# Performance work log

Hardware: AMD Instinct MI355X
Metric: run time of the kernel (lower is better)

The kernel has to match this reference:

```python
import jax, jax.numpy as jnp
import numpy as np

N = 500000
D = 112
H = 64
W = 176


def setup_inputs() -> dict:
    key = jax.random.key(0)
    k1, k2 = jax.random.split(key)
    # positions: x in [0, W-1), y in [0, H-1)
    u = jax.random.uniform(k1, (N, 2), dtype=jnp.float32)
    sampling_positions = u * jnp.array([W - 1.0, H - 1.0], dtype=jnp.float32)
    sampling_depth_features = jax.random.normal(k2, (N, D), dtype=jnp.float32)
    return {
        "sampling_positions": sampling_positions,
        "sampling_depth_features": sampling_depth_features,
        "height": H,
        "width": W,
    }


def _bilinear_scatter(positions, features, height, width):
    # positions: [N,2] (x, y); features: [N,D] -> grid [H,W,D]
    x = positions[:, 0]
    y = positions[:, 1]
    x0 = jnp.floor(x)
    y0 = jnp.floor(y)
    wx = x - x0
    wy = y - y0
    x0i = x0.astype(jnp.int32)
    y0i = y0.astype(jnp.int32)
    x1i = x0i + 1
    y1i = y0i + 1

    out = jnp.zeros((height, width, features.shape[1]), dtype=jnp.float32)

    def in_bounds(yi, xi):
        return (yi >= 0) & (yi < height) & (xi >= 0) & (xi < width)

    corners = [
        (y0i, x0i, (1.0 - wy) * (1.0 - wx)),
        (y0i, x1i, (1.0 - wy) * wx),
        (y1i, x0i, wy * (1.0 - wx)),
        (y1i, x1i, wy * wx),
    ]
    for yi, xi, w in corners:
        valid = in_bounds(yi, xi)
        w = jnp.where(valid, w, 0.0)
        yi = jnp.clip(yi, 0, height - 1)
        xi = jnp.clip(xi, 0, width - 1)
        out = out.at[yi, xi].add(w[:, None] * features)
    return out


def reference(sampling_positions, sampling_depth_features, height, width):
    return _bilinear_scatter(sampling_positions, sampling_depth_features, height, width)
```

## Files before the change

kernel.cpp:

```cpp
#include <hip/hip_runtime.h>


#define D     112
#define H     64
#define W     176
#define HW    (H * W)
#define CAP   128
#define CSTR  16
#define TY    4
#define TX    4
#define GX    (W / TX)
#define GY    (H / TY)
#define NCELL (TY * TX)

__global__ __launch_bounds__(256) void fill_kernel(
    const float2* __restrict__ pos,
    int* __restrict__ cnt,
    uint2* __restrict__ bucket,
    int N)
{
    int p = blockIdx.x * blockDim.x + threadIdx.x;
    if (p >= N) return;

    float2 xy = pos[p];
    float xf = floorf(xy.x), yf = floorf(xy.y);
    float wx = xy.x - xf,    wy = xy.y - yf;
    int x0 = (int)xf, y0 = (int)yf;
    x0 = min(max(x0, 0), W - 1);
    y0 = min(max(y0, 0), H - 1);

    int bin = y0 * W + x0;
    unsigned qw = (__float2uint_rn(wy * 65535.0f) << 16)
                |  __float2uint_rn(wx * 65535.0f);

    int i = atomicAdd(&cnt[bin * CSTR], 1);
    if (i < CAP) bucket[(size_t)bin * CAP + i] = make_uint2((unsigned)p, qw);
}

__global__ __launch_bounds__(256) void accum_kernel(
    const float* __restrict__ feat,
    const int* __restrict__ cnt,
    const uint2* __restrict__ bucket,
    float* __restrict__ out)
{
    const int tile = blockIdx.x;
    const int ty0  = (tile / GX) * TY;
    const int tx0  = (tile % GX) * TX;
    const int t    = threadIdx.x;
    const int g    = t >> 7;
    const int tl   = t & 127;

    __shared__ uint2 se[CAP];
    __shared__ float sacc[NCELL][D];

    float acc[NCELL];
#pragma unroll
    for (int c = 0; c < NCELL; ++c) acc[c] = 0.0f;

#pragma unroll
    for (int by = -1; by < TY; ++by) {
#pragma unroll
        for (int bx = -1; bx < TX; ++bx) {
            const int gby = ty0 + by;
            const int gbx = tx0 + bx;
            int n = 0;
            if (gby >= 0 && gbx >= 0 && gbx < W)
                n = min(cnt[(gby * W + gbx) * CSTR], CAP);

            if (t < n) se[t] = bucket[(size_t)(gby * W + gbx) * CAP + t];
            __syncthreads();

            if (tl < D) {
#pragma unroll 4
                for (int e = g; e < n; e += 2) {
                    uint2 en = se[e];
                    float wx = (float)(en.y & 0xffffu) * (1.0f / 65535.0f);
                    float wy = (float)(en.y >> 16)     * (1.0f / 65535.0f);
                    float f  = feat[(size_t)en.x * D + tl];
                    float ax = 1.0f - wx, ay = 1.0f - wy;
#pragma unroll
                    for (int dy = 0; dy < 2; ++dy) {
                        const int cy = by + dy;
                        if (cy < 0 || cy >= TY) continue;
                        float fy = dy ? wy : ay;
#pragma unroll
                        for (int dx = 0; dx < 2; ++dx) {
                            const int cx = bx + dx;
                            if (cx < 0 || cx >= TX) continue;
                            float fx = dx ? wx : ax;
                            acc[cy * TX + cx] = fmaf(fy * fx, f, acc[cy * TX + cx]);
                        }
                    }
                }
            }
            __syncthreads();
        }
    }

    if (g == 1 && tl < D) {
#pragma unroll
        for (int c = 0; c < NCELL; ++c) sacc[c][tl] = acc[c];
    }
    __syncthreads();
    if (g == 0 && tl < D) {
#pragma unroll
        for (int c = 0; c < NCELL; ++c) {
            const int cy = c / TX, cx = c % TX;
            out[((size_t)(ty0 + cy) * W + (tx0 + cx)) * D + tl]
                = acc[c] + sacc[c][tl];
        }
    }
}

extern "C" void kernel_launch(void* const* d_in, const int* in_sizes, int n_in,
                              void* d_out, int out_size, void* d_ws, size_t ws_size,
                              hipStream_t stream) {
    const float2* pos = (const float2*)d_in[0];
    const float* feat = (const float*)d_in[1];
    float* out        = (float*)d_out;

    const int N = in_sizes[0] / 2;

    int* cnt      = (int*)d_ws;
    uint2* bucket = (uint2*)((char*)d_ws + (size_t)HW * CSTR * sizeof(int));

    hipMemsetAsync(cnt, 0, (size_t)HW * CSTR * sizeof(int), stream);

    fill_kernel<<<(N + 255) / 256, 256, 0, stream>>>(pos, cnt, bucket, N);
    accum_kernel<<<GY * GX, 256, 0, stream>>>(feat, cnt, bucket, out);
}
```

Before: 403.9 us.

## Split bins into two sub-buckets and accumulate with 8 warps over float2 features

The fill kernel now handles two points per thread, reading positions as float4, and spreads each bin across two sub-buckets by point parity to reduce atomic contention. The accumulation kernel uses 512 threads as 8 wavefronts, each lane handling two feature channels via float2 loads, and reads bucket entries directly from global memory instead of staging them through shared memory with per-bin barriers. Partial sums are combined through a staged shared-memory reduction. This raises parallelism per tile and removes syncs, but increases register pressure (float2 accumulators for 16 cells) and memory traffic on the reduction, and the per-sub-bucket cap of 64 changes the overflow behaviour.

```diff
diff --git a/kernel.cpp b/kernel.cpp
--- a/kernel.cpp
+++ b/kernel.cpp
@@ -2,42 +2,54 @@
 
 
 #define D     112
+#define D2    56
 #define H     64
 #define W     176
 #define HW    (H * W)
-#define CAP   128
+#define S     2
+#define SCAP  64
 #define CSTR  16
 #define TY    4
 #define TX    4
 #define GX    (W / TX)
 #define GY    (H / TY)
 #define NCELL (TY * TX)
+#define NW    8
+
+__device__ __forceinline__ void fill_one(int p, float x, float y,
+                                         int* cnt, uint2* bucket)
+{
+    float xf = floorf(x), yf = floorf(y);
+    float wx = x - xf,    wy = y - yf;
+    int x0 = min(max((int)xf, 0), W - 1);
+    int y0 = min(max((int)yf, 0), H - 1);
+    int sb = (y0 * W + x0) * S + (p & 1);
+    unsigned qw = (__float2uint_rn(wy * 65535.0f) << 16)
+                |  __float2uint_rn(wx * 65535.0f);
+    int i = atomicAdd(&cnt[sb * CSTR], 1);
+    if (i < SCAP) bucket[(size_t)sb * SCAP + i] = make_uint2((unsigned)p, qw);
+}
 
 __global__ __launch_bounds__(256) void fill_kernel(
-    const float2* __restrict__ pos,
+    const float4* __restrict__ pos2,
     int* __restrict__ cnt,
     uint2* __restrict__ bucket,
     int N)
 {
-    int p = blockIdx.x * blockDim.x + threadIdx.x;
-    if (p >= N) return;
-
-    float2 xy = pos[p];
-    float xf = floorf(xy.x), yf = floorf(xy.y);
-    float wx = xy.x - xf,    wy = xy.y - yf;
-    int x0 = (int)xf, y0 = (int)yf;
-    x0 = min(max(x0, 0), W - 1);
-    y0 = min(max(y0, 0), H - 1);
-
-    int bin = y0 * W + x0;
-    unsigned qw = (__float2uint_rn(wy * 65535.0f) << 16)
-                |  __float2uint_rn(wx * 65535.0f);
-
-    int i = atomicAdd(&cnt[bin * CSTR], 1);
-    if (i < CAP) bucket[(size_t)bin * CAP + i] = make_uint2((unsigned)p, qw);
+    int i = blockIdx.x * blockDim.x + threadIdx.x;
+    int p0 = 2 * i;
+    if (p0 >= N) return;
+    if (p0 + 1 < N) {
+        float4 q = pos2[i];
+        fill_one(p0,     q.x, q.y, cnt, bucket);
+        fill_one(p0 + 1, q.z, q.w, cnt, bucket);
+    } else {
+        float2 q = ((const float2*)pos2)[p0];
+        fill_one(p0, q.x, q.y, cnt, bucket);
+    }
 }
 
-__global__ __launch_bounds__(256) void accum_kernel(
+__global__ __launch_bounds__(512, 6) void accum_kernel(
     const float* __restrict__ feat,
     const int* __restrict__ cnt,
     const uint2* __restrict__ bucket,
@@ -47,15 +59,13 @@
     const int ty0  = (tile / GX) * TY;
     const int tx0  = (tile % GX) * TX;
     const int t    = threadIdx.x;
-    const int g    = t >> 7;
-    const int tl   = t & 127;
+    const int wid  = t >> 6;
+    const int lane = t & 63;
+    const bool act = lane < D2;
 
-    __shared__ uint2 se[CAP];
-    __shared__ float sacc[NCELL][D];
-
-    float acc[NCELL];
+    float2 acc[NCELL];
 #pragma unroll
-    for (int c = 0; c < NCELL; ++c) acc[c] = 0.0f;
+    for (int c = 0; c < NCELL; ++c) acc[c] = make_float2(0.0f, 0.0f);
 
 #pragma unroll
     for (int by = -1; by < TY; ++by) {
@@ -63,51 +73,72 @@
         for (int bx = -1; bx < TX; ++bx) {
             const int gby = ty0 + by;
             const int gbx = tx0 + bx;
-            int n = 0;
-            if (gby >= 0 && gbx >= 0 && gbx < W)
-                n = min(cnt[(gby * W + gbx) * CSTR], CAP);
-
-            if (t < n) se[t] = bucket[(size_t)(gby * W + gbx) * CAP + t];
-            __syncthreads();
-
-            if (tl < D) {
-#pragma unroll 4
-                for (int e = g; e < n; e += 2) {
-                    uint2 en = se[e];
+            if (gby < 0 || gbx < 0 || gbx >= W) continue;
+            const int bin = gby * W + gbx;
+#pragma unroll
+            for (int s = 0; s < S; ++s) {
+                const int sb = bin * S + s;
+                const int n  = min(cnt[sb * CSTR], SCAP);
+                const uint2* __restrict__ bk = bucket + (size_t)sb * SCAP;
+#pragma unroll 2
+                for (int e = wid; e < n; e += NW) {
+                    uint2 en = bk[e];
                     float wx = (float)(en.y & 0xffffu) * (1.0f / 65535.0f);
                     float wy = (float)(en.y >> 16)     * (1.0f / 65535.0f);
-                    float f  = feat[(size_t)en.x * D + tl];
+                    float2 f = make_float2(0.0f, 0.0f);
+                    if (act)
+                        f = ((const float2*)(feat + (size_t)en.x * D))[lane];
                     float ax = 1.0f - wx, ay = 1.0f - wy;
 #pragma unroll
                     for (int dy = 0; dy < 2; ++dy) {
                         const int cy = by + dy;
                         if (cy < 0 || cy >= TY) continue;
-                        float fy = dy ? wy : ay;
+                        const float fy = dy ? wy : ay;
 #pragma unroll
                         for (int dx = 0; dx < 2; ++dx) {
                             const int cx = bx + dx;
                             if (cx < 0 || cx >= TX) continue;
-                            float fx = dx ? wx : ax;
-                            acc[cy * TX + cx] = fmaf(fy * fx, f, acc[cy * TX + cx]);
+                            const float fw = fy * (dx ? wx : ax);
+                            const int c = cy * TX + cx;
+                            acc[c].x = fmaf(fw, f.x, acc[c].x);
+                            acc[c].y = fmaf(fw, f.y, acc[c].y);
                         }
                     }
                 }
             }
-            __syncthreads();
         }
     }
 
-    if (g == 1 && tl < D) {
+    __shared__ float2 sacc[2][NCELL][D2];
+    const int half = wid >> 2;
+    const int sub  = wid & 3;
+
+    for (int w = 0; w < 4; ++w) {
+        if (sub == w && act) {
+            if (w == 0) {
 #pragma unroll
-        for (int c = 0; c < NCELL; ++c) sacc[c][tl] = acc[c];
+                for (int c = 0; c < NCELL; ++c) sacc[half][c][lane] = acc[c];
+            } else {
+#pragma unroll
+                for (int c = 0; c < NCELL; ++c) {
+                    float2 v = sacc[half][c][lane];
+                    v.x += acc[c].x; v.y += acc[c].y;
+                    sacc[half][c][lane] = v;
+                }
+            }
+        }
+        __syncthreads();
     }
-    __syncthreads();
-    if (g == 0 && tl < D) {
+
+    if (act) {
 #pragma unroll
-        for (int c = 0; c < NCELL; ++c) {
+        for (int k = 0; k < 2; ++k) {
+            const int c  = wid * 2 + k;
             const int cy = c / TX, cx = c % TX;
-            out[((size_t)(ty0 + cy) * W + (tx0 + cx)) * D + tl]
-                = acc[c] + sacc[c][tl];
+            float2 v0 = sacc[0][c][lane];
+            float2 v1 = sacc[1][c][lane];
+            float2* dst = (float2*)(out + ((size_t)(ty0 + cy) * W + (tx0 + cx)) * D);
+            dst[lane] = make_float2(v0.x + v1.x, v0.y + v1.y);
         }
     }
 }
@@ -115,17 +146,19 @@
 extern "C" void kernel_launch(void* const* d_in, const int* in_sizes, int n_in,
                               void* d_out, int out_size, void* d_ws, size_t ws_size,
                               hipStream_t stream) {
-    const float2* pos = (const float2*)d_in[0];
-    const float* feat = (const float*)d_in[1];
-    float* out        = (float*)d_out;
+    const float4* pos2 = (const float4*)d_in[0];
+    const float* feat  = (const float*)d_in[1];
+    float* out         = (float*)d_out;
 
     const int N = in_sizes[0] / 2;
 
     int* cnt      = (int*)d_ws;
-    uint2* bucket = (uint2*)((char*)d_ws + (size_t)HW * CSTR * sizeof(int));
+    uint2* bucket = (uint2*)((char*)d_ws + (size_t)HW * S * CSTR * sizeof(int));
 
-    hipMemsetAsync(cnt, 0, (size_t)HW * CSTR * sizeof(int), stream);
+    hipMemsetAsync(cnt, 0, (size_t)HW * S * CSTR * sizeof(int), stream);
 
-    fill_kernel<<<(N + 255) / 256, 256, 0, stream>>>(pos, cnt, bucket, N);
-    accum_kernel<<<GY * GX, 256, 0, stream>>>(feat, cnt, bucket, out);
+    int npair = (N + 1) / 2;
+    fill_kernel<<<(npair + 255) / 256, 256, 0, stream>>>(pos2, cnt, bucket, N);
+
+    accum_kernel<<<GY * GX, 512, 0, stream>>>(feat, cnt, bucket, out);
 }
```

Measured after the change: 426.5 us. +5.6%, slower.
